# Kernel optimization log

Hardware: AMD Instinct MI355X
Metric: run time of the kernel (lower is better)

## Reference

```python
import jax, jax.numpy as jnp
import numpy as np

N, M, D = 8192, 8192, 64


def setup_inputs() -> dict:
    key = jax.random.key(0)
    kx, ky, kg = jax.random.split(key, 3)
    x = jax.random.normal(kx, (N, D), dtype=jnp.float32)
    y = jax.random.normal(ky, (M, D), dtype=jnp.float32)
    # per-dimension gamma (anisotropic branch: gamma.numel() == d), positive
    gamma = jax.random.uniform(kg, (D,), dtype=jnp.float32, minval=0.1, maxval=2.0)
    return {"x": x, "y": y, "gamma": gamma}


def reference(x, y, gamma):
    # k(x, y) = exp(-sum_i gamma_i * (x_i - y_i)^2)
    # Fused form: gamma-weighted squared distance via the expansion
    # avoids materializing the (n, m, d) broadcast tensor.
    sq_x = jnp.sum(gamma * x * x, axis=-1)          # (n,)
    sq_y = jnp.sum(gamma * y * y, axis=-1)          # (m,)
    cross = jnp.einsum('nd,md->nm', x, gamma * y)   # (n, m)
    norm = sq_x[:, None] + sq_y[None, :] - 2.0 * cross
    return jnp.exp(-norm)
```

## Files before the change

### kernel.cpp

```cpp
#include <hip/hip_runtime.h>
#include <hip/hip_bf16.h>
#include <stdint.h>


#define KPAD 136
#define CSTRIDE 68

typedef __attribute__((ext_vector_type(8))) short bfrag8;
typedef __attribute__((ext_vector_type(4))) float facc4;
typedef __attribute__((ext_vector_type(4))) float f32x4;

__device__ __forceinline__ unsigned short f2bf(float v) {
  uint32_t u = __float_as_uint(v);
  u += 0x7fffu + ((u >> 16) & 1u);
  return (unsigned short)(u >> 16);
}
__device__ __forceinline__ float bf2f(unsigned short h) {
  return __uint_as_float(((uint32_t)h) << 16);
}

__global__ __launch_bounds__(256)
void qkm_prep(const float* __restrict__ x, const float* __restrict__ y,
              const float* __restrict__ gamma,
              unsigned short* __restrict__ Apack, unsigned short* __restrict__ Bpack,
              float* __restrict__ sqx, float* __restrict__ sqy, int N, int M) {
  const int t = blockIdx.x * blockDim.x + threadIdx.x;
  const bool isB = (t >= N);
  const int r = isB ? (t - N) : t;
  if (isB && r >= M) return;
  const float4* src = (const float4*)((isB ? y : x) + (size_t)r * 64);
  const float4* gv = (const float4*)gamma;
  unsigned short* dst = isB ? Bpack : Apack;

  unsigned short hi[64], lo[64];
  float s = 0.f;
#pragma unroll
  for (int c = 0; c < 16; ++c) {
    const float4 v = src[c];
    const float4 g4 = gv[c];
    const float vj[4] = {v.x, v.y, v.z, v.w};
    const float gj[4] = {g4.x, g4.y, g4.z, g4.w};
#pragma unroll
    for (int j = 0; j < 4; ++j) {
      const float val = vj[j];
      s = fmaf(gj[j] * val, val, s);
      const float wv = isB ? (2.f * gj[j] * val) : val;
      const unsigned short h = f2bf(wv);
      hi[c * 4 + j] = h;
      lo[c * 4 + j] = f2bf(wv - bf2f(h));
    }
  }
  (isB ? sqy : sqx)[r] = s;

  const int p = r >> 4, lr = r & 15;
#pragma unroll
  for (int kb = 0; kb < 4; ++kb) {
#pragma unroll
    for (int lq = 0; lq < 4; ++lq) {
      unsigned short tmp[8];
#pragma unroll
      for (int j = 0; j < 8; ++j) {
        const int kk = kb * 32 + lq * 8 + j;
        tmp[j] = (kk < 64) ? hi[kk] : lo[kk - 64];
      }
      uint4 pk;
      pk.x = (uint32_t)tmp[0] | ((uint32_t)tmp[1] << 16);
      pk.y = (uint32_t)tmp[2] | ((uint32_t)tmp[3] << 16);
      pk.z = (uint32_t)tmp[4] | ((uint32_t)tmp[5] << 16);
      pk.w = (uint32_t)tmp[6] | ((uint32_t)tmp[7] << 16);
      *(uint4*)&dst[(((size_t)(p * 4 + kb)) * 64 + lq * 16 + lr) * 8] = pk;
    }
  }
}

__global__ __launch_bounds__(256, 4)
void qkm_main(const unsigned short* __restrict__ Apack,
              const unsigned short* __restrict__ Bpack,
              const float* __restrict__ sqx, const float* __restrict__ sqy,
              float* __restrict__ out, int M) {
  __shared__ __align__(16) float Ct[64 * CSTRIDE];

  const int tid = threadIdx.x;
  const int l = tid & 63, wv = tid >> 6;
  const int n0 = blockIdx.y * 64, m0 = blockIdx.x * 64;
  const int rb = (wv & 1) * 32, cb = (wv >> 1) * 32;
  const int lr = l & 15, lq = l >> 4;

  const unsigned short* Af = Apack + (((size_t)((n0 + rb) >> 4) * 4) * 64 + l) * 8;
  const unsigned short* Bf = Bpack + (((size_t)((m0 + cb) >> 4) * 4) * 64 + l) * 8;

  bfrag8 a[2][4], b[2][4];
#pragma unroll
  for (int dp = 0; dp < 2; ++dp)
#pragma unroll
    for (int kb = 0; kb < 4; ++kb) {
      a[dp][kb] = *(const bfrag8*)(Af + (size_t)(dp * 4 + kb) * 512);
      b[dp][kb] = *(const bfrag8*)(Bf + (size_t)(dp * 4 + kb) * 512);
    }

  facc4 acc[2][2] = {};
  const int ka[6] = {0, 1, 0, 1, 2, 3};
  const int kc[6] = {0, 1, 2, 3, 0, 1};
#pragma unroll
  for (int s = 0; s < 6; ++s) {
#pragma unroll
    for (int dp = 0; dp < 2; ++dp)
#pragma unroll
      for (int dq = 0; dq < 2; ++dq)
        acc[dp][dq] = __builtin_amdgcn_mfma_f32_16x16x32_bf16(
            a[dp][ka[s]], b[dq][kc[s]], acc[dp][dq], 0, 0, 0);
  }

  const float sy0 = sqy[m0 + cb + lr];
  const float sy1 = sqy[m0 + cb + 16 + lr];
#pragma unroll
  for (int ti = 0; ti < 2; ++ti) {
    const int rloc = rb + ti * 16 + lq * 4;
    const float4 sx = *(const float4*)&sqx[n0 + rloc];
    const float sxa[4] = {sx.x, sx.y, sx.z, sx.w};
#pragma unroll
    for (int q = 0; q < 4; ++q) {
      float* crow = Ct + (size_t)(rloc + q) * CSTRIDE;
      crow[cb + lr]      = __expf(acc[ti][0][q] - sxa[q] - sy0);
      crow[cb + 16 + lr] = __expf(acc[ti][1][q] - sxa[q] - sy1);
    }
  }
  __syncthreads();

#pragma unroll
  for (int i = 0; i < 4; ++i) {
    const int f = tid + 256 * i;
    const int row = f >> 4;
    const int c4 = f & 15;
    const f32x4 v = *(const f32x4*)(Ct + row * CSTRIDE + c4 * 4);
    __builtin_nontemporal_store(v, (f32x4*)(out + (size_t)(n0 + row) * M + m0 + c4 * 4));
  }
}

__global__ __launch_bounds__(256, 4)
void qkm_rbf_fallback(const float* __restrict__ x, const float* __restrict__ y,
                      const float* __restrict__ gamma, float* __restrict__ out,
                      int M) {
  __shared__ __align__(16) unsigned short Ah[64 * KPAD];
  __shared__ __align__(16) unsigned short Bh[64 * KPAD];
  __shared__ float sqx[64];
  __shared__ float sqy[64];

  const int tid = threadIdx.x;
  const int n0 = blockIdx.y * 64;
  const int m0 = blockIdx.x * 64;
  {
    const float4* xv = (const float4*)(x + (size_t)n0 * 64);
    const float4* yv = (const float4*)(y + (size_t)m0 * 64);
    const float4* gv = (const float4*)gamma;
#pragma unroll
    for (int i = 0; i < 4; ++i) {
      const int f = tid + 256 * i;
      const int r = f >> 4;
      const int c = f & 15;
      const float4 g4 = gv[c];
      const float gj[4] = {g4.x, g4.y, g4.z, g4.w};
      {
        const float4 v = xv[f];
        const float vj[4] = {v.x, v.y, v.z, v.w};
        unsigned short h[4], lo[4];
        float s = 0.f;
#pragma unroll
        for (int j = 0; j < 4; ++j) {
          const float xval = vj[j];
          h[j] = f2bf(xval);
          lo[j] = f2bf(xval - bf2f(h[j]));
          s = fmaf(gj[j] * xval, xval, s);
        }
        uint2 hp, lp;
        hp.x = (uint32_t)h[0] | ((uint32_t)h[1] << 16);
        hp.y = (uint32_t)h[2] | ((uint32_t)h[3] << 16);
        lp.x = (uint32_t)lo[0] | ((uint32_t)lo[1] << 16);
        lp.y = (uint32_t)lo[2] | ((uint32_t)lo[3] << 16);
        *(uint2*)&Ah[r * KPAD + c * 4]      = hp;
        *(uint2*)&Ah[r * KPAD + 64 + c * 4] = lp;
        s += __shfl_xor(s, 1); s += __shfl_xor(s, 2);
        s += __shfl_xor(s, 4); s += __shfl_xor(s, 8);
        if (c == 0) sqx[r] = s;
      }
      {
        const float4 v = yv[f];
        const float vj[4] = {v.x, v.y, v.z, v.w};
        unsigned short h[4], lo[4];
        float s = 0.f;
#pragma unroll
        for (int j = 0; j < 4; ++j) {
          const float yval = vj[j];
          const float w = 2.f * gj[j] * yval;
          h[j] = f2bf(w);
          lo[j] = f2bf(w - bf2f(h[j]));
          s = fmaf(gj[j] * yval, yval, s);
        }
        uint2 hp, lp;
        hp.x = (uint32_t)h[0] | ((uint32_t)h[1] << 16);
        hp.y = (uint32_t)h[2] | ((uint32_t)h[3] << 16);
        lp.x = (uint32_t)lo[0] | ((uint32_t)lo[1] << 16);
        lp.y = (uint32_t)lo[2] | ((uint32_t)lo[3] << 16);
        *(uint2*)&Bh[r * KPAD + c * 4]      = hp;
        *(uint2*)&Bh[r * KPAD + 64 + c * 4] = lp;
        s += __shfl_xor(s, 1); s += __shfl_xor(s, 2);
        s += __shfl_xor(s, 4); s += __shfl_xor(s, 8);
        if (c == 0) sqy[r] = s;
      }
    }
  }
  __syncthreads();

  const int l = tid & 63;
  const int wv = tid >> 6;
  const int rb = (wv & 1) * 32;
  const int cb = (wv >> 1) * 32;
  const int lr = l & 15;
  const int lq = l >> 4;

  facc4 acc[2][2] = {};
  const unsigned short* A0 = &Ah[(rb + lr) * KPAD + lq * 8];
  const unsigned short* A1 = A0 + 16 * KPAD;
  const unsigned short* B0 = &Bh[(cb + lr) * KPAD + lq * 8];
  const unsigned short* B1 = B0 + 16 * KPAD;
  const int akb[6] = {0, 32, 0, 32, 64, 96};
  const int bkb[6] = {0, 32, 64, 96, 0, 32};
#pragma unroll
  for (int p = 0; p < 6; ++p) {
    bfrag8 a0 = *(const bfrag8*)(A0 + akb[p]);
    bfrag8 a1 = *(const bfrag8*)(A1 + akb[p]);
    bfrag8 b0 = *(const bfrag8*)(B0 + bkb[p]);
    bfrag8 b1 = *(const bfrag8*)(B1 + bkb[p]);
    acc[0][0] = __builtin_amdgcn_mfma_f32_16x16x32_bf16(a0, b0, acc[0][0], 0, 0, 0);
    acc[0][1] = __builtin_amdgcn_mfma_f32_16x16x32_bf16(a0, b1, acc[0][1], 0, 0, 0);
    acc[1][0] = __builtin_amdgcn_mfma_f32_16x16x32_bf16(a1, b0, acc[1][0], 0, 0, 0);
    acc[1][1] = __builtin_amdgcn_mfma_f32_16x16x32_bf16(a1, b1, acc[1][1], 0, 0, 0);
  }
  __syncthreads();

  float* Ct = (float*)Ah;
  const float sy0 = sqy[cb + lr];
  const float sy1 = sqy[cb + 16 + lr];
#pragma unroll
  for (int ti = 0; ti < 2; ++ti) {
    const int rloc = rb + ti * 16 + lq * 4;
    const float4 sx = *(const float4*)&sqx[rloc];
    const float sxa[4] = {sx.x, sx.y, sx.z, sx.w};
#pragma unroll
    for (int q = 0; q < 4; ++q) {
      float* crow = Ct + (size_t)(rloc + q) * CSTRIDE;
      crow[cb + lr]      = __expf(acc[ti][0][q] - sxa[q] - sy0);
      crow[cb + 16 + lr] = __expf(acc[ti][1][q] - sxa[q] - sy1);
    }
  }
  __syncthreads();
#pragma unroll
  for (int i = 0; i < 4; ++i) {
    const int f = tid + 256 * i;
    const int row = f >> 4;
    const int c4 = f & 15;
    const float4 v = *(const float4*)(Ct + row * CSTRIDE + c4 * 4);
    *(float4*)(out + (size_t)(n0 + row) * M + m0 + c4 * 4) = v;
  }
}

extern "C" void kernel_launch(void* const* d_in, const int* in_sizes, int n_in,
                              void* d_out, int out_size, void* d_ws, size_t ws_size,
                              hipStream_t stream) {
  const float* x = (const float*)d_in[0];
  const float* y = (const float*)d_in[1];
  const float* g = (const float*)d_in[2];
  float* out = (float*)d_out;
  const int D = in_sizes[2];
  const int N = in_sizes[0] / D;
  const int M = in_sizes[1] / D;

  const size_t aBytes = (size_t)N * 128 * sizeof(unsigned short);
  const size_t bBytes = (size_t)M * 128 * sizeof(unsigned short);
  const size_t sxBytes = (size_t)N * sizeof(float);
  const size_t syBytes = (size_t)M * sizeof(float);
  const size_t need = aBytes + bBytes + sxBytes + syBytes + 256;

  if (ws_size >= need) {
    char* ws = (char*)d_ws;
    unsigned short* Apack = (unsigned short*)ws;
    unsigned short* Bpack = (unsigned short*)(ws + aBytes);
    float* sqx = (float*)(ws + aBytes + bBytes);
    float* sqy = (float*)(ws + aBytes + bBytes + sxBytes);
    qkm_prep<<<(N + M + 255) / 256, 256, 0, stream>>>(x, y, g, Apack, Bpack, sqx, sqy, N, M);
    dim3 grid(M / 64, N / 64);
    qkm_main<<<grid, dim3(256), 0, stream>>>(Apack, Bpack, sqx, sqy, out, M);
  } else {
    dim3 grid(M / 64, N / 64);
    qkm_rbf_fallback<<<grid, dim3(256), 0, stream>>>(x, y, g, out, M);
  }
}
```

Before: 278.5 us.

## Retile main kernel to 16x256 output tiles with each wave owning 64 columns

Changes the main kernel tile from 64x64 to 16 rows by 256 columns. All four waves now share one A row block and each computes four 16x16 column tiles. Each output row segment becomes 1 KB of contiguous stores, and the B fragments are loaded in two halves to reduce register pressure. In exchange, each wave now fetches more B data per output element.

```diff
diff --git a/kernel.cpp b/kernel.cpp
--- a/kernel.cpp
+++ b/kernel.cpp
@@ -5,6 +5,7 @@
 
 #define KPAD 136
 #define CSTRIDE 68
+#define C2STRIDE 260
 
 typedef __attribute__((ext_vector_type(8))) short bfrag8;
 typedef __attribute__((ext_vector_type(4))) float facc4;
@@ -78,61 +79,69 @@
               const unsigned short* __restrict__ Bpack,
               const float* __restrict__ sqx, const float* __restrict__ sqy,
               float* __restrict__ out, int M) {
-  __shared__ __align__(16) float Ct[64 * CSTRIDE];
+  __shared__ __align__(16) float Ct[16 * C2STRIDE];
 
   const int tid = threadIdx.x;
   const int l = tid & 63, wv = tid >> 6;
-  const int n0 = blockIdx.y * 64, m0 = blockIdx.x * 64;
-  const int rb = (wv & 1) * 32, cb = (wv >> 1) * 32;
+  const int n0 = blockIdx.y * 16, m0 = blockIdx.x * 256;
   const int lr = l & 15, lq = l >> 4;
 
-  const unsigned short* Af = Apack + (((size_t)((n0 + rb) >> 4) * 4) * 64 + l) * 8;
-  const unsigned short* Bf = Bpack + (((size_t)((m0 + cb) >> 4) * 4) * 64 + l) * 8;
-
-  bfrag8 a[2][4], b[2][4];
-#pragma unroll
-  for (int dp = 0; dp < 2; ++dp)
-#pragma unroll
-    for (int kb = 0; kb < 4; ++kb) {
-      a[dp][kb] = *(const bfrag8*)(Af + (size_t)(dp * 4 + kb) * 512);
-      b[dp][kb] = *(const bfrag8*)(Bf + (size_t)(dp * 4 + kb) * 512);
-    }
-
-  facc4 acc[2][2] = {};
-  const int ka[6] = {0, 1, 0, 1, 2, 3};
-  const int kc[6] = {0, 1, 2, 3, 0, 1};
-#pragma unroll
-  for (int s = 0; s < 6; ++s) {
-#pragma unroll
-    for (int dp = 0; dp < 2; ++dp)
-#pragma unroll
-      for (int dq = 0; dq < 2; ++dq)
-        acc[dp][dq] = __builtin_amdgcn_mfma_f32_16x16x32_bf16(
-            a[dp][ka[s]], b[dq][kc[s]], acc[dp][dq], 0, 0, 0);
-  }
-
-  const float sy0 = sqy[m0 + cb + lr];
-  const float sy1 = sqy[m0 + cb + 16 + lr];
-#pragma unroll
-  for (int ti = 0; ti < 2; ++ti) {
-    const int rloc = rb + ti * 16 + lq * 4;
-    const float4 sx = *(const float4*)&sqx[n0 + rloc];
-    const float sxa[4] = {sx.x, sx.y, sx.z, sx.w};
-#pragma unroll
-    for (int q = 0; q < 4; ++q) {
-      float* crow = Ct + (size_t)(rloc + q) * CSTRIDE;
-      crow[cb + lr]      = __expf(acc[ti][0][q] - sxa[q] - sy0);
-      crow[cb + 16 + lr] = __expf(acc[ti][1][q] - sxa[q] - sy1);
-    }
+  const unsigned short* Af = Apack + ((size_t)(n0 >> 4) * 4 * 64 + l) * 8;
+  const unsigned short* Bf = Bpack + ((size_t)((m0 >> 4) + wv * 4) * 4 * 64 + l) * 8;
+
+  facc4 acc[4] = {};
+  bfrag8 aH[2], aT[2], bT[4][2];
+
+#pragma unroll
+  for (int k = 0; k < 2; ++k) aH[k] = *(const bfrag8*)(Af + (size_t)k * 512);
+#pragma unroll
+  for (int ct = 0; ct < 4; ++ct)
+#pragma unroll
+    for (int k = 0; k < 2; ++k)
+      bT[ct][k] = *(const bfrag8*)(Bf + ((size_t)ct * 4 + k) * 512);
+#pragma unroll
+  for (int k = 0; k < 2; ++k)
+#pragma unroll
+    for (int ct = 0; ct < 4; ++ct)
+      acc[ct] = __builtin_amdgcn_mfma_f32_16x16x32_bf16(aH[k], bT[ct][k], acc[ct], 0, 0, 0);
+
+#pragma unroll
+  for (int k = 0; k < 2; ++k) aT[k] = *(const bfrag8*)(Af + (size_t)(2 + k) * 512);
+#pragma unroll
+  for (int k = 0; k < 2; ++k)
+#pragma unroll
+    for (int ct = 0; ct < 4; ++ct)
+      acc[ct] = __builtin_amdgcn_mfma_f32_16x16x32_bf16(aT[k], bT[ct][k], acc[ct], 0, 0, 0);
+
+#pragma unroll
+  for (int ct = 0; ct < 4; ++ct)
+#pragma unroll
+    for (int k = 0; k < 2; ++k)
+      bT[ct][k] = *(const bfrag8*)(Bf + ((size_t)ct * 4 + 2 + k) * 512);
+#pragma unroll
+  for (int k = 0; k < 2; ++k)
+#pragma unroll
+    for (int ct = 0; ct < 4; ++ct)
+      acc[ct] = __builtin_amdgcn_mfma_f32_16x16x32_bf16(aH[k], bT[ct][k], acc[ct], 0, 0, 0);
+
+  const float4 sx = *(const float4*)&sqx[n0 + lq * 4];
+  const float sxa[4] = {sx.x, sx.y, sx.z, sx.w};
+#pragma unroll
+  for (int ct = 0; ct < 4; ++ct) {
+    const int col = wv * 64 + ct * 16 + lr;
+    const float sy = sqy[m0 + col];
+#pragma unroll
+    for (int q = 0; q < 4; ++q)
+      Ct[(lq * 4 + q) * C2STRIDE + col] = __expf(acc[ct][q] - sxa[q] - sy);
   }
   __syncthreads();
 
 #pragma unroll
   for (int i = 0; i < 4; ++i) {
     const int f = tid + 256 * i;
-    const int row = f >> 4;
-    const int c4 = f & 15;
-    const f32x4 v = *(const f32x4*)(Ct + row * CSTRIDE + c4 * 4);
+    const int row = f >> 6;
+    const int c4 = f & 63;
+    const f32x4 v = *(const f32x4*)(Ct + row * C2STRIDE + c4 * 4);
     __builtin_nontemporal_store(v, (f32x4*)(out + (size_t)(n0 + row) * M + m0 + c4 * 4));
   }
 }
@@ -288,7 +297,7 @@
     float* sqx = (float*)(ws + aBytes + bBytes);
     float* sqy = (float*)(ws + aBytes + bBytes + sxBytes);
     qkm_prep<<<(N + M + 255) / 256, 256, 0, stream>>>(x, y, g, Apack, Bpack, sqx, sqy, N, M);
-    dim3 grid(M / 64, N / 64);
+    dim3 grid(M / 256, N / 16);
     qkm_main<<<grid, dim3(256), 0, stream>>>(Apack, Bpack, sqx, sqy, out, M);
   } else {
     dim3 grid(M / 64, N / 64);
```

Measured after the change: 285.3 us. 1.02x slower.
